# Performance work log

Hardware: AMD Instinct MI355X
Metric: run time of the kernel (lower is better)

## Reference

```python
import jax, jax.numpy as jnp
import numpy as np

D = 2048      # attn_dim
H = 16        # num_heads
HD = D // H   # head_dim = 128
FF = 8192     # ffn_dim
BASE = 10000.0
EPS = 1e-6


def setup_inputs() -> dict:
    key = jax.random.key(0)
    ks = jax.random.split(key, 10)
    b, t = 2, 2048
    s = 1.0 / np.sqrt(D)
    x = jax.random.normal(ks[0], (b, t, D), dtype=jnp.float32)
    position_ids = jnp.arange(b * t, dtype=jnp.int64).reshape(b, t)  # values < maxlen=4096
    return {
        "x": x,
        "position_ids": position_ids,
        "Wq": jax.random.normal(ks[1], (D, D), jnp.float32) * s,
        "Wk": jax.random.normal(ks[2], (D, D), jnp.float32) * s,
        "Wv": jax.random.normal(ks[3], (D, D), jnp.float32) * s,
        "Wo": jax.random.normal(ks[4], (D, D), jnp.float32) * s,
        "Wg": jax.random.normal(ks[5], (D, FF), jnp.float32) * s,
        "Wu": jax.random.normal(ks[6], (D, FF), jnp.float32) * s,
        "Wd": jax.random.normal(ks[7], (FF, D), jnp.float32) * (1.0 / np.sqrt(FF)),
        "g1": jnp.ones((D,), jnp.float32),
        "g2": jnp.ones((D,), jnp.float32),
    }


def _rmsnorm(x, g):
    return x * jax.lax.rsqrt(jnp.mean(x * x, axis=-1, keepdims=True) + EPS) * g


def _rope_cos_sin(position_ids):
    # get_cos_sin: theta over even dims, then repeat(1, 2) -> (b, t, HD)
    inv_freq = 1.0 / (BASE ** (jnp.arange(0, HD, 2, dtype=jnp.float32) / HD))
    ang = position_ids[..., None].astype(jnp.float32) * inv_freq  # (b, t, HD/2)
    cos = jnp.concatenate([jnp.cos(ang), jnp.cos(ang)], axis=-1)  # (b, t, HD)
    sin = jnp.concatenate([jnp.sin(ang), jnp.sin(ang)], axis=-1)
    return cos, sin


def _rotate_half(x):
    x1, x2 = x[..., : HD // 2], x[..., HD // 2:]
    return jnp.concatenate([-x2, x1], axis=-1)


def _attention(xn, position_ids, Wq, Wk, Wv, Wo):
    b, t, _ = xn.shape
    q = (xn @ Wq).reshape(b, t, H, HD).transpose(0, 2, 1, 3)  # b h t d
    k = (xn @ Wk).reshape(b, t, H, HD).transpose(0, 2, 1, 3)
    v = (xn @ Wv).reshape(b, t, H, HD).transpose(0, 2, 1, 3)
    cos, sin = _rope_cos_sin(position_ids)
    cos = cos[:, None]  # b 1 t d
    sin = sin[:, None]
    q = q * cos + _rotate_half(q) * sin
    k = k * cos + _rotate_half(k) * sin
    scores = jnp.einsum("bhqd,bhkd->bhqk", q, k) / np.sqrt(HD).astype(np.float32)
    causal = jnp.triu(jnp.ones((t, t), dtype=bool), k=1)  # True above diagonal
    scores = jnp.where(causal, jnp.float32(-10000.0), scores)
    attn = jax.nn.softmax(scores, axis=-1)
    o = jnp.einsum("bhqk,bhkd->bhqd", attn, v)
    o = o.transpose(0, 2, 1, 3).reshape(b, t, D)
    return o @ Wo


def reference(x, position_ids, Wq, Wk, Wv, Wo, Wg, Wu, Wd, g1, g2):
    x = x + _attention(_rmsnorm(x, g1), position_ids, Wq, Wk, Wv, Wo)
    h = _rmsnorm(x, g2)
    x = x + (jax.nn.silu(h @ Wg) * (h @ Wu)) @ Wd
    return x
```

## Files before the change

kernel.cpp:

```cpp
#include <hip/hip_runtime.h>
#include <cstdint>

#define D_  2048
#define H_  16
#define HD_ 128
#define FF_ 8192
#define T_  2048
#define B_  2
#define BT_ (B_*T_)
#define NP_ (B_*H_)
#define QKVLD_ (3*D_)

typedef __attribute__((ext_vector_type(8))) _Float16 half8;
typedef __attribute__((ext_vector_type(4))) float   floatx4;

__device__ __forceinline__ void gl_lds16(const void* g, void* l) {
  __builtin_amdgcn_global_load_lds(
      (const __attribute__((address_space(1))) void*)(uintptr_t)g,
      (__attribute__((address_space(3))) void*)(uintptr_t)l,
      16, 0, 0);
}

__global__ void wconv_kernel(const float* __restrict__ W, _Float16* __restrict__ Wt,
                             int K, int N) {
  __shared__ float tile[64][33];
  int n0 = blockIdx.x * 32, k0 = blockIdx.y * 64;
  int tx = threadIdx.x, ty = threadIdx.y;
#pragma unroll
  for (int r = 0; r < 64; r += 8)
    tile[ty + r][tx] = W[(size_t)(k0 + ty + r) * N + n0 + tx];
  __syncthreads();
#pragma unroll
  for (int r = 0; r < 32; r += 8) {
    float a = tile[tx * 2][ty + r], b = tile[tx * 2 + 1][ty + r];
    union { _Float16 h[2]; unsigned u; } cv;
    cv.h[0] = (_Float16)a; cv.h[1] = (_Float16)b;
    ((unsigned*)(Wt + (size_t)(n0 + ty + r) * K + k0))[tx] = cv.u;
  }
}

__global__ void rmsnorm_kernel(const float* __restrict__ x, const float* __restrict__ g,
                               _Float16* __restrict__ out) {
  int row = blockIdx.x, tid = threadIdx.x;
  const float4* xr = (const float4*)(x + (size_t)row * D_);
  float4 v1 = xr[tid], v2 = xr[tid + 256];
  float ss = v1.x*v1.x + v1.y*v1.y + v1.z*v1.z + v1.w*v1.w
           + v2.x*v2.x + v2.y*v2.y + v2.z*v2.z + v2.w*v2.w;
  __shared__ float red[256];
  red[tid] = ss; __syncthreads();
  for (int s = 128; s > 0; s >>= 1) { if (tid < s) red[tid] += red[tid + s]; __syncthreads(); }
  float rs = rsqrtf(red[0] * (1.0f / D_) + 1e-6f);
  float4 ga = ((const float4*)g)[tid], gb = ((const float4*)g)[tid + 256];
  _Float16* orow = out + (size_t)row * D_;
  _Float16 t[4] __attribute__((aligned(8)));
  t[0] = (_Float16)(v1.x * rs * ga.x);
  t[1] = (_Float16)(v1.y * rs * ga.y);
  t[2] = (_Float16)(v1.z * rs * ga.z);
  t[3] = (_Float16)(v1.w * rs * ga.w);
  *(uint2*)(orow + tid * 4) = *(const uint2*)t;
  t[0] = (_Float16)(v2.x * rs * gb.x);
  t[1] = (_Float16)(v2.y * rs * gb.y);
  t[2] = (_Float16)(v2.z * rs * gb.z);
  t[3] = (_Float16)(v2.w * rs * gb.w);
  *(uint2*)(orow + (tid + 256) * 4) = *(const uint2*)t;
}

template<int OUTMODE>
__global__ __launch_bounds__(512, 2) void gemm256(
    const _Float16* __restrict__ A, const _Float16* __restrict__ Bt,
    void* __restrict__ Cv, const float* __restrict__ Res,
    int M, int N, int K, int lda, int ldb, int ldc)
{
  extern __shared__ _Float16 smem[];

  const int gx = gridDim.x, gy = gridDim.y, gz = gridDim.z;
  int pid = (blockIdx.z * gy + blockIdx.y) * gx + blockIdx.x;
  const int qch = (gx * gy * gz) >> 3;
  int lid = (pid & 7) * qch + (pid >> 3);
  const int bx = lid % gx; lid /= gx;
  const int by = lid % gy; const int bz = lid / gy;

  const int tid  = threadIdx.x;
  const int lane = tid & 63;
  const int w    = tid >> 6;
  const int wm   = w >> 2;
  const int wn   = w & 3;
  const int l15  = lane & 15, q4 = lane >> 4;
  const int m0   = by * 256;
  const int n0   = bx * 256;
  const int KP   = K / gz;
  const int koff = bz * KP;
  const int NT   = KP >> 6;

  const int srow8  = lane >> 3;
  const int schunk = (((lane & 7) ^ (srow8 & 7)) << 3);
  const _Float16* AgP = A  + (size_t)(m0 + w * 8 + srow8) * lda + schunk + koff;
  const _Float16* BgP = Bt + (size_t)(n0 + w * 8 + srow8) * ldb + schunk + koff;
  const int ldsW = w * 512;

  const int c0 = ((q4 ^ (l15 & 7)) << 3);
  const int c1 = c0 ^ 32;
  const int arow_e = (wm * 128 + l15) * 64;
  const int brow_e = (wn * 64 + l15) * 64;
  const _Float16* aB[2][2];
  const _Float16* bB[2][2];
  aB[0][0] = smem + arow_e + c0;          aB[0][1] = smem + arow_e + c1;
  aB[1][0] = aB[0][0] + 32768;            aB[1][1] = aB[0][1] + 32768;
  bB[0][0] = smem + 16384 + brow_e + c0;  bB[0][1] = smem + 16384 + brow_e + c1;
  bB[1][0] = bB[0][0] + 32768;            bB[1][1] = bB[0][1] + 32768;

  floatx4 acc[8][4];
#pragma unroll
  for (int i = 0; i < 8; ++i)
#pragma unroll
    for (int j = 0; j < 4; ++j)
#pragma unroll
      for (int r = 0; r < 4; ++r) acc[i][j][r] = 0.0f;

  half8 bf[2][4];
  half8 af0[4], af1[4];

#define STA(S, h, s, KO)                                                     \
  gl_lds16(AgP + (size_t)((h) * 128 + (s) * 64) * lda + (KO),                \
           smem + (S) * 32768 + (h) * 8192 + (s) * 4096 + ldsW)
#define STB(S, h, s, KO)                                                     \
  gl_lds16(BgP + (size_t)((h) * 128 + (s) * 64) * ldb + (KO),                \
           smem + (S) * 32768 + 16384 + (h) * 8192 + (s) * 4096 + ldsW)

#define SB0   __builtin_amdgcn_sched_barrier(0)
#define BARR  __builtin_amdgcn_s_barrier()
#define LGKM0 asm volatile("s_waitcnt lgkmcnt(0)" ::: "memory")

#define RD_B8(S)                                                             \
  { _Pragma("unroll")                                                        \
    for (int j = 0; j < 4; ++j) {                                            \
      bf[0][j] = *(const half8*)(bB[S][0] + j * 1024);                       \
      bf[1][j] = *(const half8*)(bB[S][1] + j * 1024);                       \
    } }
#define RD_A4(S, q, af)                                                      \
  { _Pragma("unroll")                                                        \
    for (int i2 = 0; i2 < 2; ++i2) {                                         \
      af[i2*2+0] = *(const half8*)(aB[S][0] + ((q)*2+i2) * 1024);            \
      af[i2*2+1] = *(const half8*)(aB[S][1] + ((q)*2+i2) * 1024);            \
    } }
#define MFMA_Q(q, af)                                                        \
  { _Pragma("unroll")                                                        \
    for (int kk = 0; kk < 2; ++kk)                                           \
      _Pragma("unroll")                                                      \
      for (int i2 = 0; i2 < 2; ++i2)                                         \
        _Pragma("unroll")                                                    \
        for (int j = 0; j < 4; ++j)                                          \
          acc[(q)*2+i2][j] = __builtin_amdgcn_mfma_f32_16x16x32_f16(         \
              af[i2*2+kk], bf[kk][j], acc[(q)*2+i2][j], 0, 0, 0);            \
  }

#define TILE(S, t, KOA, KOB)                                                 \
  {                                                                          \
    const bool s1 = (t) + 1 < NT, s2 = (t) + 2 < NT;                         \
                                                   \
    RD_B8(S); RD_A4(S, 0, af0);                                              \
    if (s1) { STA((S) ^ 1, 0, 0, KOA); STA((S) ^ 1, 0, 1, KOA); }            \
    asm volatile("s_waitcnt lgkmcnt(8)" ::: "memory");                       \
    SB0; BARR; LGKM0; SB0;                                                   \
    __builtin_amdgcn_s_setprio(1); MFMA_Q(0, af0); __builtin_amdgcn_s_setprio(0); \
    SB0; BARR;                                                               \
                                                           \
    RD_A4(S, 1, af1);                                                        \
    if (s1) { STA((S) ^ 1, 1, 0, KOA); STA((S) ^ 1, 1, 1, KOA); }            \
    SB0; BARR; LGKM0; SB0;                                                   \
    __builtin_amdgcn_s_setprio(1); MFMA_Q(1, af1); __builtin_amdgcn_s_setprio(0); \
    SB0; BARR;                                                               \
                                                           \
    RD_A4(S, 2, af0);                                                        \
    if (s2) { STB(S, 0, 0, KOB); STB(S, 0, 1, KOB); }                        \
    SB0; BARR; LGKM0; SB0;                                                   \
    __builtin_amdgcn_s_setprio(1); MFMA_Q(2, af0); __builtin_amdgcn_s_setprio(0); \
    SB0; BARR;                                                               \
                                                           \
    RD_A4(S, 3, af1);                                                        \
    if (s2) { STB(S, 1, 0, KOB); STB(S, 1, 1, KOB); }                        \
    SB0; BARR; LGKM0; SB0;                                                   \
    __builtin_amdgcn_s_setprio(1); MFMA_Q(3, af1); __builtin_amdgcn_s_setprio(0); \
    SB0;                                                                     \
    if (s2)      asm volatile("s_waitcnt vmcnt(4)" ::: "memory");            \
    else if (s1) asm volatile("s_waitcnt vmcnt(0)" ::: "memory");            \
    BARR;                                                                    \
  }

  STA(0, 0, 0, 0); STA(0, 0, 1, 0); STA(0, 1, 0, 0); STA(0, 1, 1, 0);
  STB(0, 0, 0, 0); STB(0, 0, 1, 0); STB(0, 1, 0, 0); STB(0, 1, 1, 0);
  if (NT > 1) {
    STB(1, 0, 0, 64); STB(1, 0, 1, 64); STB(1, 1, 0, 64); STB(1, 1, 1, 64);
    asm volatile("s_waitcnt vmcnt(4)" ::: "memory");
  } else {
    asm volatile("s_waitcnt vmcnt(0)" ::: "memory");
  }
  BARR;

  for (int t = 0; t < NT; t += 2) {
    TILE(0, t,     64, 128);
    TILE(1, t + 1, 128, 192);
    AgP += 128; BgP += 128;
  }

#undef STA
#undef STB
#undef SB0
#undef BARR
#undef LGKM0
#undef RD_B8
#undef RD_A4
#undef MFMA_Q
#undef TILE

  const int crow0 = m0 + wm * 128 + q4 * 4;
  const int ccol0 = n0 + wn * 64 + l15;
#pragma unroll
  for (int i = 0; i < 8; ++i)
#pragma unroll
    for (int j = 0; j < 4; ++j)
#pragma unroll
      for (int r = 0; r < 4; ++r) {
        size_t o = (size_t)(crow0 + i * 16 + r) * ldc + (ccol0 + j * 16);
        if constexpr (OUTMODE == 0)      ((_Float16*)Cv)[o] = (_Float16)acc[i][j][r];
        else if constexpr (OUTMODE == 1) ((float*)Cv)[o] = acc[i][j][r] + Res[o];
        else ((float*)Cv)[(size_t)bz * M * ldc + o] = acc[i][j][r];
      }
}

__global__ void addred_kernel(const float* __restrict__ parts, const float* __restrict__ res,
                              float* __restrict__ out) {
  size_t i = ((size_t)blockIdx.x * 256 + threadIdx.x) * 4;
  const size_t MN = (size_t)BT_ * D_;
  float4 a = *(const float4*)(parts + i);
  float4 b = *(const float4*)(parts + MN + i);
  float4 r = *(const float4*)(res + i);
  float4 o;
  o.x = a.x + b.x + r.x; o.y = a.y + b.y + r.y;
  o.z = a.z + b.z + r.z; o.w = a.w + b.w + r.w;
  *(float4*)(out + i) = o;
}

__global__ __launch_bounds__(256, 2) void fattn_kernel(
    const _Float16* __restrict__ qkv, const _Float16* __restrict__ vt,
    _Float16* __restrict__ ob)
{
  __shared__ _Float16 Pl[128 * 136];
  const int pr = blockIdx.x;
  const int yq = blockIdx.y;
  const int b = pr >> 4, h = pr & 15;
  const int lane = threadIdx.x & 63, w = threadIdx.x >> 6;
  const int l15 = lane & 15, q4 = lane >> 4;
  const float scale = 0.08838834764831845f;

  const _Float16* qg = qkv + (size_t)b * T_ * QKVLD_ + (size_t)h * HD_;
  const _Float16* kg = qg + D_;
  const _Float16* vg = vt + (size_t)pr * HD_ * T_;
  _Float16* og = ob + (size_t)b * T_ * D_ + (size_t)h * HD_;

  for (int hf = 0; hf < 2; ++hf) {
    const int qb = hf ? (15 - yq) : yq;
    const int qrow0 = qb * 128 + w * 32;

    half8 qf[2][4];
#pragma unroll
    for (int i = 0; i < 2; ++i)
#pragma unroll
      for (int kf = 0; kf < 4; ++kf)
        qf[i][kf] = *(const half8*)(qg + (size_t)(qrow0 + i * 16 + l15) * QKVLD_
                                       + kf * 32 + q4 * 8);

    floatx4 Oa[2][8];
    float m[8], l[8];
#pragma unroll
    for (int i = 0; i < 2; ++i)
#pragma unroll
      for (int j = 0; j < 8; ++j)
#pragma unroll
        for (int r = 0; r < 4; ++r) Oa[i][j][r] = 0.f;
#pragma unroll
    for (int z = 0; z < 8; ++z) { m[z] = -1e30f; l[z] = 0.f; }

    for (int kt = 0; kt <= qb; ++kt) {
      floatx4 s[2][8];
#pragma unroll
      for (int i = 0; i < 2; ++i)
#pragma unroll
        for (int j = 0; j < 8; ++j)
#pragma unroll
          for (int r = 0; r < 4; ++r) s[i][j][r] = 0.f;
#pragma unroll
      for (int kf = 0; kf < 4; ++kf) {
#pragma unroll
        for (int j = 0; j < 8; ++j) {
          half8 kf8 = *(const half8*)(kg + (size_t)(kt * 128 + j * 16 + l15) * QKVLD_
                                         + kf * 32 + q4 * 8);
          s[0][j] = __builtin_amdgcn_mfma_f32_16x16x32_f16(qf[0][kf], kf8, s[0][j], 0, 0, 0);
          s[1][j] = __builtin_amdgcn_mfma_f32_16x16x32_f16(qf[1][kf], kf8, s[1][j], 0, 0, 0);
        }
      }
#pragma unroll
      for (int i = 0; i < 2; ++i)
#pragma unroll
        for (int j = 0; j < 8; ++j)
#pragma unroll
          for (int r = 0; r < 4; ++r) s[i][j][r] *= scale;
      if (kt == qb) {
#pragma unroll
        for (int i = 0; i < 2; ++i)
#pragma unroll
          for (int j = 0; j < 8; ++j)
#pragma unroll
            for (int r = 0; r < 4; ++r)
              if (j * 16 + l15 > w * 32 + i * 16 + q4 * 4 + r) s[i][j][r] = -1e30f;
      }
#pragma unroll
      for (int i = 0; i < 2; ++i)
#pragma unroll
        for (int r = 0; r < 4; ++r) {
          const int z = i * 4 + r;
          float pm = s[i][0][r];
#pragma unroll
          for (int j = 1; j < 8; ++j) pm = fmaxf(pm, s[i][j][r]);
          pm = fmaxf(pm, __shfl_xor(pm, 1));
          pm = fmaxf(pm, __shfl_xor(pm, 2));
          pm = fmaxf(pm, __shfl_xor(pm, 4));
          pm = fmaxf(pm, __shfl_xor(pm, 8));
          float mn = fmaxf(m[z], pm);
          float sc = __expf(m[z] - mn);
          m[z] = mn;
          float ls = 0.f;
#pragma unroll
          for (int j = 0; j < 8; ++j) {
            float e = __expf(s[i][j][r] - mn);
            s[i][j][r] = e;
            ls += e;
          }
          ls += __shfl_xor(ls, 1);
          ls += __shfl_xor(ls, 2);
          ls += __shfl_xor(ls, 4);
          ls += __shfl_xor(ls, 8);
          l[z] = l[z] * sc + ls;
#pragma unroll
          for (int jd = 0; jd < 8; ++jd) Oa[i][jd][r] *= sc;
        }
#pragma unroll
      for (int i = 0; i < 2; ++i)
#pragma unroll
        for (int r = 0; r < 4; ++r) {
          _Float16* prow = &Pl[(size_t)(w * 32 + i * 16 + q4 * 4 + r) * 136 + l15];
#pragma unroll
          for (int j = 0; j < 8; ++j) prow[j * 16] = (_Float16)s[i][j][r];
        }
#pragma unroll
      for (int ks = 0; ks < 4; ++ks) {
        half8 pf0 = *(const half8*)&Pl[(size_t)(w * 32 + l15) * 136 + ks * 32 + q4 * 8];
        half8 pf1 = *(const half8*)&Pl[(size_t)(w * 32 + 16 + l15) * 136 + ks * 32 + q4 * 8];
#pragma unroll
        for (int jd = 0; jd < 8; ++jd) {
          half8 vf = *(const half8*)(vg + (size_t)(jd * 16 + l15) * T_
                                        + kt * 128 + ks * 32 + q4 * 8);
          Oa[0][jd] = __builtin_amdgcn_mfma_f32_16x16x32_f16(pf0, vf, Oa[0][jd], 0, 0, 0);
          Oa[1][jd] = __builtin_amdgcn_mfma_f32_16x16x32_f16(pf1, vf, Oa[1][jd], 0, 0, 0);
        }
      }
    }
#pragma unroll
    for (int i = 0; i < 2; ++i)
#pragma unroll
      for (int r = 0; r < 4; ++r) {
        float inv = 1.0f / l[i * 4 + r];
        _Float16* orow = og + (size_t)(qrow0 + i * 16 + q4 * 4 + r) * D_;
#pragma unroll
        for (int jd = 0; jd < 8; ++jd)
          orow[jd * 16 + l15] = (_Float16)(Oa[i][jd][r] * inv);
      }
  }
}

__global__ void rope_kernel(_Float16* __restrict__ qkv, const void* __restrict__ pos) {
  int gid = blockIdx.x * 256 + threadIdx.x;
  int d = gid & 63;
  int h = (gid >> 6) & 15;
  int bt = gid >> 10;
  const int* pi = (const int*)pos;
  long long pv = (pi[1] == 0 && pi[2] == 1) ? ((const long long*)pos)[bt]
                                            : (long long)pi[bt];
  float inv = exp2f((float)d * -0.2076205059304601f);
  float ang = (float)pv * inv;
  float s, c;
  sincosf(ang, &s, &c);
  size_t base = (size_t)bt * QKVLD_ + (size_t)h * HD_ + d;
  _Float16* q = qkv;
  _Float16* k = qkv + D_;
  float x1v = (float)q[base], x2v = (float)q[base + 64];
  q[base]      = (_Float16)(x1v * c - x2v * s);
  q[base + 64] = (_Float16)(x2v * c + x1v * s);
  x1v = (float)k[base]; x2v = (float)k[base + 64];
  k[base]      = (_Float16)(x1v * c - x2v * s);
  k[base + 64] = (_Float16)(x2v * c + x1v * s);
}

__global__ void vtrans_kernel(const _Float16* __restrict__ v, _Float16* __restrict__ vt,
                              int ld) {
  __shared__ _Float16 tile[32][33];
  int t0 = blockIdx.x * 32, d0 = blockIdx.y * 32, bh = blockIdx.z;
  int b = bh >> 4, h = bh & 15;
  int tx = threadIdx.x, ty = threadIdx.y;
  const _Float16* vb = v + (size_t)b * T_ * ld + (size_t)h * HD_;
#pragma unroll
  for (int r = 0; r < 32; r += 8)
    tile[ty + r][tx] = vb[(size_t)(t0 + ty + r) * ld + d0 + tx];
  __syncthreads();
  _Float16* vo = vt + ((size_t)bh * HD_ + d0) * T_ + t0;
#pragma unroll
  for (int r = 0; r < 32; r += 8)
    vo[(size_t)(ty + r) * T_ + tx] = tile[tx][ty + r];
}

__global__ void silumul_kernel(_Float16* __restrict__ gate, const _Float16* __restrict__ up) {
  size_t idx = ((size_t)blockIdx.x * 256 + threadIdx.x) * 8;
  uint4 gr = *(const uint4*)(gate + idx);
  uint4 ur = *(const uint4*)(up + idx);
  const _Float16* gh = (const _Float16*)&gr;
  const _Float16* uh = (const _Float16*)&ur;
  _Float16 t[8] __attribute__((aligned(16)));
#pragma unroll
  for (int l = 0; l < 8; l++) {
    float x = (float)gh[l];
    float s = x / (1.0f + __expf(-x));
    t[l] = (_Float16)(s * (float)uh[l]);
  }
  *(uint4*)(gate + idx) = *(const uint4*)t;
}

extern "C" void kernel_launch(void* const* d_in, const int* in_sizes, int n_in,
                              void* d_out, int out_size, void* d_ws, size_t ws_size,
                              hipStream_t stream) {
  (void)in_sizes; (void)n_in; (void)out_size;
  const float* x   = (const float*)d_in[0];
  const void*  pos = d_in[1];
  const float* W[7] = { (const float*)d_in[2], (const float*)d_in[3],
                        (const float*)d_in[4], (const float*)d_in[5],
                        (const float*)d_in[6], (const float*)d_in[7],
                        (const float*)d_in[8] };
  const float* g1  = (const float*)d_in[9];
  const float* g2  = (const float*)d_in[10];
  float* out = (float*)d_out;

  const int wk[7] = { D_, D_, D_, D_, D_, D_, FF_ };
  const int wn[7] = { D_, D_, D_, D_, FF_, FF_, D_ };

  char* p = (char*)d_ws;
  auto carve = [&](size_t bytes) { char* r = p; p += (bytes + 255) & ~(size_t)255; return r; };

  _Float16* scratch = (_Float16*)carve((size_t)64 * 1024 * 1024);
  const size_t FLAT_NEED = (size_t)336 * 1024 * 1024;
  bool flat = ws_size >= FLAT_NEED;
  _Float16* w16[7];
  if (flat) {
    for (int i = 0; i < 7; i++) w16[i] = (_Float16*)carve((size_t)wk[i] * wn[i] * 2);
  } else {
    _Float16* wslot = (_Float16*)carve((size_t)D_ * FF_ * 2);
    w16[0] = wslot;
    w16[1] = wslot + (size_t)D_ * D_;
    w16[2] = wslot + (size_t)2 * D_ * D_;
    w16[3] = w16[4] = w16[5] = w16[6] = wslot;
  }
  _Float16* qkv = (_Float16*)carve((size_t)BT_ * QKVLD_ * 2);
  _Float16* ob  = (_Float16*)carve((size_t)BT_ * D_ * 2);
  _Float16* xn  = (_Float16*)carve((size_t)BT_ * D_ * 2);
  _Float16* vt  = (_Float16*)carve((size_t)BT_ * D_ * 2);
  float*    x1  = (float*)   carve((size_t)BT_ * D_ * 4);
  _Float16* gate = scratch;
  _Float16* up   = qkv;
  _Float16* hb   = xn;
  float* oparts = (float*)scratch;
  float* dparts = (float*)qkv;

  dim3 b328(32, 8);
  auto conv = [&](int i) {
    wconv_kernel<<<dim3(wn[i] / 32, wk[i] / 64), b328, 0, stream>>>(W[i], w16[i], wk[i], wn[i]);
  };
  if (flat) for (int i = 0; i < 7; i++) conv(i);

  rmsnorm_kernel<<<BT_, 256, 0, stream>>>(x, g1, xn);

  if (!flat) { conv(0); conv(1); conv(2); }
  gemm256<0><<<dim3(QKVLD_ / 256, BT_ / 256, 1), 512, 131072, stream>>>(
      xn, w16[0], qkv, nullptr, BT_, QKVLD_, D_, D_, D_, QKVLD_);

  rope_kernel<<<(BT_ * H_ * 64) / 256, 256, 0, stream>>>(qkv, pos);

  vtrans_kernel<<<dim3(T_ / 32, HD_ / 32, NP_), b328, 0, stream>>>(qkv + 2 * D_, vt, QKVLD_);

  fattn_kernel<<<dim3(NP_, 8), 256, 0, stream>>>(qkv, vt, ob);

  if (!flat) conv(3);
  gemm256<2><<<dim3(D_ / 256, BT_ / 256, 2), 512, 131072, stream>>>(
      ob, w16[3], oparts, nullptr, BT_, D_, D_, D_, D_, D_);
  addred_kernel<<<(BT_ * D_ / 4) / 256, 256, 0, stream>>>(oparts, x, x1);

  rmsnorm_kernel<<<BT_, 256, 0, stream>>>(x1, g2, hb);

  if (!flat) conv(4);
  gemm256<0><<<dim3(FF_ / 256, BT_ / 256, 1), 512, 131072, stream>>>(
      hb, w16[4], gate, nullptr, BT_, FF_, D_, D_, D_, FF_);
  if (!flat) conv(5);
  gemm256<0><<<dim3(FF_ / 256, BT_ / 256, 1), 512, 131072, stream>>>(
      hb, w16[5], up, nullptr, BT_, FF_, D_, D_, D_, FF_);

  silumul_kernel<<<(BT_ * FF_ / 8) / 256, 256, 0, stream>>>(gate, up);

  if (!flat) conv(6);
  gemm256<2><<<dim3(D_ / 256, BT_ / 256, 2), 512, 131072, stream>>>(
      gate, w16[6], dparts, nullptr, BT_, D_, FF_, FF_, FF_, D_);
  addred_kernel<<<(BT_ * D_ / 4) / 256, 256, 0, stream>>>(dparts, x1, out);
}
```

Baseline: 1.179 ms.

## Split attention q-blocks across blocks and double-buffer K/V register loads

Each attention workgroup now handles a single 128-row query block instead of a causal-balanced pair. This doubles the grid to 16 blocks in y (512 workgroups) for more parallelism on the GPU. The K and V fragment loads are software-pipelined into two register buffers, so the next k-slice is fetched while the current MFMAs run, hiding global-load latency. The cost is higher register pressure from the extra half8 buffers, which may reduce occupancy, and uneven per-block work under the causal mask.

```diff
diff --git a/kernel.cpp b/kernel.cpp
--- a/kernel.cpp
+++ b/kernel.cpp
@@ -248,6 +248,7 @@
   __shared__ _Float16 Pl[128 * 136];
   const int pr = blockIdx.x;
   const int yq = blockIdx.y;
+  const int qb = (yq < 8) ? yq : 23 - yq;
   const int b = pr >> 4, h = pr & 15;
   const int lane = threadIdx.x & 63, w = threadIdx.x >> 6;
   const int l15 = lane & 15, q4 = lane >> 4;
@@ -258,124 +259,143 @@
   const _Float16* vg = vt + (size_t)pr * HD_ * T_;
   _Float16* og = ob + (size_t)b * T_ * D_ + (size_t)h * HD_;
 
-  for (int hf = 0; hf < 2; ++hf) {
-    const int qb = hf ? (15 - yq) : yq;
-    const int qrow0 = qb * 128 + w * 32;
-
-    half8 qf[2][4];
+  const int qrow0 = qb * 128 + w * 32;
+
+  half8 qf[2][4];
+#pragma unroll
+  for (int i = 0; i < 2; ++i)
+#pragma unroll
+    for (int kf = 0; kf < 4; ++kf)
+      qf[i][kf] = *(const half8*)(qg + (size_t)(qrow0 + i * 16 + l15) * QKVLD_
+                                     + kf * 32 + q4 * 8);
+
+  floatx4 Oa[2][8];
+  float m[8], l[8];
+#pragma unroll
+  for (int i = 0; i < 2; ++i)
+#pragma unroll
+    for (int j = 0; j < 8; ++j)
+#pragma unroll
+      for (int r = 0; r < 4; ++r) Oa[i][j][r] = 0.f;
+#pragma unroll
+  for (int z = 0; z < 8; ++z) { m[z] = -1e30f; l[z] = 0.f; }
+
+  for (int kt = 0; kt <= qb; ++kt) {
+    const _Float16* kb_ = kg + (size_t)(kt * 128 + l15) * QKVLD_ + q4 * 8;
+    half8 k0[8], k1[8];
+#pragma unroll
+    for (int j = 0; j < 8; ++j)
+      k0[j] = *(const half8*)(kb_ + (size_t)(j * 16) * QKVLD_);
+    floatx4 s[2][8];
 #pragma unroll
     for (int i = 0; i < 2; ++i)
 #pragma unroll
-      for (int kf = 0; kf < 4; ++kf)
-        qf[i][kf] = *(const half8*)(qg + (size_t)(qrow0 + i * 16 + l15) * QKVLD_
-                                       + kf * 32 + q4 * 8);
-
-    floatx4 Oa[2][8];
-    float m[8], l[8];
+      for (int j = 0; j < 8; ++j)
+#pragma unroll
+        for (int r = 0; r < 4; ++r) s[i][j][r] = 0.f;
+#pragma unroll
+    for (int kf = 0; kf < 4; ++kf) {
+      if (kf < 3) {
+#pragma unroll
+        for (int j = 0; j < 8; ++j) {
+          half8 nx = *(const half8*)(kb_ + (size_t)(j * 16) * QKVLD_ + (kf + 1) * 32);
+          if (kf & 1) k0[j] = nx; else k1[j] = nx;
+        }
+      }
+#pragma unroll
+      for (int j = 0; j < 8; ++j) {
+        half8 cur = (kf & 1) ? k1[j] : k0[j];
+        s[0][j] = __builtin_amdgcn_mfma_f32_16x16x32_f16(qf[0][kf], cur, s[0][j], 0, 0, 0);
+        s[1][j] = __builtin_amdgcn_mfma_f32_16x16x32_f16(qf[1][kf], cur, s[1][j], 0, 0, 0);
+      }
+    }
 #pragma unroll
     for (int i = 0; i < 2; ++i)
 #pragma unroll
       for (int j = 0; j < 8; ++j)
 #pragma unroll
-        for (int r = 0; r < 4; ++r) Oa[i][j][r] = 0.f;
-#pragma unroll
-    for (int z = 0; z < 8; ++z) { m[z] = -1e30f; l[z] = 0.f; }
-
-    for (int kt = 0; kt <= qb; ++kt) {
-      floatx4 s[2][8];
+        for (int r = 0; r < 4; ++r) s[i][j][r] *= scale;
+    if (kt == qb) {
 #pragma unroll
       for (int i = 0; i < 2; ++i)
 #pragma unroll
         for (int j = 0; j < 8; ++j)
 #pragma unroll
-          for (int r = 0; r < 4; ++r) s[i][j][r] = 0.f;
-#pragma unroll
-      for (int kf = 0; kf < 4; ++kf) {
+          for (int r = 0; r < 4; ++r)
+            if (j * 16 + l15 > w * 32 + i * 16 + q4 * 4 + r) s[i][j][r] = -1e30f;
+    }
+    const _Float16* vb_ = vg + (size_t)(l15) * T_ + kt * 128 + q4 * 8;
+    half8 v0[8], v1[8];
+#pragma unroll
+    for (int jd = 0; jd < 8; ++jd)
+      v0[jd] = *(const half8*)(vb_ + (size_t)(jd * 16) * T_);
+#pragma unroll
+    for (int i = 0; i < 2; ++i)
+#pragma unroll
+      for (int r = 0; r < 4; ++r) {
+        const int z = i * 4 + r;
+        float pm = s[i][0][r];
+#pragma unroll
+        for (int j = 1; j < 8; ++j) pm = fmaxf(pm, s[i][j][r]);
+        pm = fmaxf(pm, __shfl_xor(pm, 1));
+        pm = fmaxf(pm, __shfl_xor(pm, 2));
+        pm = fmaxf(pm, __shfl_xor(pm, 4));
+        pm = fmaxf(pm, __shfl_xor(pm, 8));
+        float mn = fmaxf(m[z], pm);
+        float sc = __expf(m[z] - mn);
+        m[z] = mn;
+        float ls = 0.f;
 #pragma unroll
         for (int j = 0; j < 8; ++j) {
-          half8 kf8 = *(const half8*)(kg + (size_t)(kt * 128 + j * 16 + l15) * QKVLD_
-                                         + kf * 32 + q4 * 8);
-          s[0][j] = __builtin_amdgcn_mfma_f32_16x16x32_f16(qf[0][kf], kf8, s[0][j], 0, 0, 0);
-          s[1][j] = __builtin_amdgcn_mfma_f32_16x16x32_f16(qf[1][kf], kf8, s[1][j], 0, 0, 0);
+          float e = __expf(s[i][j][r] - mn);
+          s[i][j][r] = e;
+          ls += e;
         }
-      }
-#pragma unroll
-      for (int i = 0; i < 2; ++i)
-#pragma unroll
-        for (int j = 0; j < 8; ++j)
-#pragma unroll
-          for (int r = 0; r < 4; ++r) s[i][j][r] *= scale;
-      if (kt == qb) {
-#pragma unroll
-        for (int i = 0; i < 2; ++i)
-#pragma unroll
-          for (int j = 0; j < 8; ++j)
-#pragma unroll
-            for (int r = 0; r < 4; ++r)
-              if (j * 16 + l15 > w * 32 + i * 16 + q4 * 4 + r) s[i][j][r] = -1e30f;
-      }
-#pragma unroll
-      for (int i = 0; i < 2; ++i)
-#pragma unroll
-        for (int r = 0; r < 4; ++r) {
-          const int z = i * 4 + r;
-          float pm = s[i][0][r];
-#pragma unroll
-          for (int j = 1; j < 8; ++j) pm = fmaxf(pm, s[i][j][r]);
-          pm = fmaxf(pm, __shfl_xor(pm, 1));
-          pm = fmaxf(pm, __shfl_xor(pm, 2));
-          pm = fmaxf(pm, __shfl_xor(pm, 4));
-          pm = fmaxf(pm, __shfl_xor(pm, 8));
-          float mn = fmaxf(m[z], pm);
-          float sc = __expf(m[z] - mn);
-          m[z] = mn;
-          float ls = 0.f;
-#pragma unroll
-          for (int j = 0; j < 8; ++j) {
-            float e = __expf(s[i][j][r] - mn);
-            s[i][j][r] = e;
-            ls += e;
-          }
-          ls += __shfl_xor(ls, 1);
-          ls += __shfl_xor(ls, 2);
-          ls += __shfl_xor(ls, 4);
-          ls += __shfl_xor(ls, 8);
-          l[z] = l[z] * sc + ls;
-#pragma unroll
-          for (int jd = 0; jd < 8; ++jd) Oa[i][jd][r] *= sc;
+        ls += __shfl_xor(ls, 1);
+        ls += __shfl_xor(ls, 2);
+        ls += __shfl_xor(ls, 4);
+        ls += __shfl_xor(ls, 8);
+        l[z] = l[z] * sc + ls;
+#pragma unroll
+        for (int jd = 0; jd < 8; ++jd) Oa[i][jd][r] *= sc;
+      }
+#pragma unroll
+    for (int i = 0; i < 2; ++i)
+#pragma unroll
+      for (int r = 0; r < 4; ++r) {
+        _Float16* prow = &Pl[(size_t)(w * 32 + i * 16 + q4 * 4 + r) * 136 + l15];
+#pragma unroll
+        for (int j = 0; j < 8; ++j) prow[j * 16] = (_Float16)s[i][j][r];
+      }
+#pragma unroll
+    for (int ks = 0; ks < 4; ++ks) {
+      if (ks < 3) {
+#pragma unroll
+        for (int jd = 0; jd < 8; ++jd) {
+          half8 nx = *(const half8*)(vb_ + (size_t)(jd * 16) * T_ + (ks + 1) * 32);
+          if (ks & 1) v0[jd] = nx; else v1[jd] = nx;
         }
-#pragma unroll
-      for (int i = 0; i < 2; ++i)
-#pragma unroll
-        for (int r = 0; r < 4; ++r) {
-          _Float16* prow = &Pl[(size_t)(w * 32 + i * 16 + q4 * 4 + r) * 136 + l15];
-#pragma unroll
-          for (int j = 0; j < 8; ++j) prow[j * 16] = (_Float16)s[i][j][r];
-        }
-#pragma unroll
-      for (int ks = 0; ks < 4; ++ks) {
-        half8 pf0 = *(const half8*)&Pl[(size_t)(w * 32 + l15) * 136 + ks * 32 + q4 * 8];
-        half8 pf1 = *(const half8*)&Pl[(size_t)(w * 32 + 16 + l15) * 136 + ks * 32 + q4 * 8];
-#pragma unroll
-        for (int jd = 0; jd < 8; ++jd) {
-          half8 vf = *(const half8*)(vg + (size_t)(jd * 16 + l15) * T_
-                                        + kt * 128 + ks * 32 + q4 * 8);
-          Oa[0][jd] = __builtin_amdgcn_mfma_f32_16x16x32_f16(pf0, vf, Oa[0][jd], 0, 0, 0);
-          Oa[1][jd] = __builtin_amdgcn_mfma_f32_16x16x32_f16(pf1, vf, Oa[1][jd], 0, 0, 0);
-        }
+      }
+      half8 pf0 = *(const half8*)&Pl[(size_t)(w * 32 + l15) * 136 + ks * 32 + q4 * 8];
+      half8 pf1 = *(const half8*)&Pl[(size_t)(w * 32 + 16 + l15) * 136 + ks * 32 + q4 * 8];
+#pragma unroll
+      for (int jd = 0; jd < 8; ++jd) {
+        half8 vf = (ks & 1) ? v1[jd] : v0[jd];
+        Oa[0][jd] = __builtin_amdgcn_mfma_f32_16x16x32_f16(pf0, vf, Oa[0][jd], 0, 0, 0);
+        Oa[1][jd] = __builtin_amdgcn_mfma_f32_16x16x32_f16(pf1, vf, Oa[1][jd], 0, 0, 0);
       }
     }
-#pragma unroll
-    for (int i = 0; i < 2; ++i)
-#pragma unroll
-      for (int r = 0; r < 4; ++r) {
-        float inv = 1.0f / l[i * 4 + r];
-        _Float16* orow = og + (size_t)(qrow0 + i * 16 + q4 * 4 + r) * D_;
-#pragma unroll
-        for (int jd = 0; jd < 8; ++jd)
-          orow[jd * 16 + l15] = (_Float16)(Oa[i][jd][r] * inv);
-      }
-  }
+  }
+#pragma unroll
+  for (int i = 0; i < 2; ++i)
+#pragma unroll
+    for (int r = 0; r < 4; ++r) {
+      float inv = 1.0f / l[i * 4 + r];
+      _Float16* orow = og + (size_t)(qrow0 + i * 16 + q4 * 4 + r) * D_;
+#pragma unroll
+      for (int jd = 0; jd < 8; ++jd)
+        orow[jd * 16 + l15] = (_Float16)(Oa[i][jd][r] * inv);
+    }
 }
 
 __global__ void rope_kernel(_Float16* __restrict__ qkv, const void* __restrict__ pos) {
@@ -494,7 +514,7 @@
 
   vtrans_kernel<<<dim3(T_ / 32, HD_ / 32, NP_), b328, 0, stream>>>(qkv + 2 * D_, vt, QKVLD_);
 
-  fattn_kernel<<<dim3(NP_, 8), 256, 0, stream>>>(qkv, vt, ob);
+  fattn_kernel<<<dim3(NP_, 16), 256, 0, stream>>>(qkv, vt, ob);
 
   if (!flat) conv(3);
   gemm256<2><<<dim3(D_ / 256, BT_ / 256, 2), 512, 131072, stream>>>(
```

Result: faster. 1.134 ms (-3.8%).

## Restructure flash attention into 64-row query blocks with software-prefetched K/V fragments

Applied to the files above, without the earlier changes.

The attention kernel now gives each block 64 query rows (16 per wave) instead of pairing two 128-row blocks, and launches 32 query blocks per head-batch pair, heaviest first. Per-thread register state is halved so launch bounds can allow 4 blocks per CU. K and V fragments are prefetched in two halves so global loads overlap with the MFMAs. K/V tiles are still re-read from global memory per block, so total K/V traffic doubles in exchange for more parallelism and occupancy.

```diff
diff --git a/kernel.cpp b/kernel.cpp
--- a/kernel.cpp
+++ b/kernel.cpp
@@ -241,13 +241,14 @@
   *(float4*)(out + i) = o;
 }
 
-__global__ __launch_bounds__(256, 2) void fattn_kernel(
+__global__ __launch_bounds__(256, 4) void fattn_kernel(
     const _Float16* __restrict__ qkv, const _Float16* __restrict__ vt,
     _Float16* __restrict__ ob)
 {
-  __shared__ _Float16 Pl[128 * 136];
+  __shared__ _Float16 Pl[64 * 136];
   const int pr = blockIdx.x;
-  const int yq = blockIdx.y;
+  const int qb = 31 - (int)blockIdx.y;
+  const int nt = (qb + 2) >> 1;
   const int b = pr >> 4, h = pr & 15;
   const int lane = threadIdx.x & 63, w = threadIdx.x >> 6;
   const int l15 = lane & 15, q4 = lane >> 4;
@@ -258,123 +259,125 @@
   const _Float16* vg = vt + (size_t)pr * HD_ * T_;
   _Float16* og = ob + (size_t)b * T_ * D_ + (size_t)h * HD_;
 
-  for (int hf = 0; hf < 2; ++hf) {
-    const int qb = hf ? (15 - yq) : yq;
-    const int qrow0 = qb * 128 + w * 32;
-
-    half8 qf[2][4];
-#pragma unroll
-    for (int i = 0; i < 2; ++i)
-#pragma unroll
-      for (int kf = 0; kf < 4; ++kf)
-        qf[i][kf] = *(const half8*)(qg + (size_t)(qrow0 + i * 16 + l15) * QKVLD_
-                                       + kf * 32 + q4 * 8);
-
-    floatx4 Oa[2][8];
-    float m[8], l[8];
-#pragma unroll
-    for (int i = 0; i < 2; ++i)
+  const int qrow0 = qb * 64 + w * 16;
+
+  half8 qf[4];
+#pragma unroll
+  for (int kf = 0; kf < 4; ++kf)
+    qf[kf] = *(const half8*)(qg + (size_t)(qrow0 + l15) * QKVLD_ + kf * 32 + q4 * 8);
+
+  floatx4 Oa[8];
+  float m[4], l[4];
+#pragma unroll
+  for (int j = 0; j < 8; ++j)
+#pragma unroll
+    for (int r = 0; r < 4; ++r) Oa[j][r] = 0.f;
+#pragma unroll
+  for (int z = 0; z < 4; ++z) { m[z] = -1e30f; l[z] = 0.f; }
+
+  for (int kt = 0; kt < nt; ++kt) {
+    const _Float16* kb_ = kg + (size_t)(kt * 128 + l15) * QKVLD_ + q4 * 8;
+    half8 ka[4], kc[4];
+#pragma unroll
+    for (int j = 0; j < 4; ++j)
+      ka[j] = *(const half8*)(kb_ + (size_t)(j * 16) * QKVLD_);
+    floatx4 s[8];
+#pragma unroll
+    for (int j = 0; j < 8; ++j)
+#pragma unroll
+      for (int r = 0; r < 4; ++r) s[j][r] = 0.f;
+#pragma unroll
+    for (int kf = 0; kf < 4; ++kf) {
+#pragma unroll
+      for (int j = 0; j < 4; ++j)
+        kc[j] = *(const half8*)(kb_ + (size_t)((j + 4) * 16) * QKVLD_ + kf * 32);
+#pragma unroll
+      for (int j = 0; j < 4; ++j)
+        s[j] = __builtin_amdgcn_mfma_f32_16x16x32_f16(qf[kf], ka[j], s[j], 0, 0, 0);
+      if (kf < 3) {
+#pragma unroll
+        for (int j = 0; j < 4; ++j)
+          ka[j] = *(const half8*)(kb_ + (size_t)(j * 16) * QKVLD_ + (kf + 1) * 32);
+      }
+#pragma unroll
+      for (int j = 0; j < 4; ++j)
+        s[4 + j] = __builtin_amdgcn_mfma_f32_16x16x32_f16(qf[kf], kc[j], s[4 + j], 0, 0, 0);
+    }
+#pragma unroll
+    for (int j = 0; j < 8; ++j)
+#pragma unroll
+      for (int r = 0; r < 4; ++r) s[j][r] *= scale;
+    if (kt == nt - 1) {
 #pragma unroll
       for (int j = 0; j < 8; ++j)
 #pragma unroll
-        for (int r = 0; r < 4; ++r) Oa[i][j][r] = 0.f;
-#pragma unroll
-    for (int z = 0; z < 8; ++z) { m[z] = -1e30f; l[z] = 0.f; }
-
-    for (int kt = 0; kt <= qb; ++kt) {
-      floatx4 s[2][8];
-#pragma unroll
-      for (int i = 0; i < 2; ++i)
-#pragma unroll
-        for (int j = 0; j < 8; ++j)
-#pragma unroll
-          for (int r = 0; r < 4; ++r) s[i][j][r] = 0.f;
-#pragma unroll
-      for (int kf = 0; kf < 4; ++kf) {
-#pragma unroll
-        for (int j = 0; j < 8; ++j) {
-          half8 kf8 = *(const half8*)(kg + (size_t)(kt * 128 + j * 16 + l15) * QKVLD_
-                                         + kf * 32 + q4 * 8);
-          s[0][j] = __builtin_amdgcn_mfma_f32_16x16x32_f16(qf[0][kf], kf8, s[0][j], 0, 0, 0);
-          s[1][j] = __builtin_amdgcn_mfma_f32_16x16x32_f16(qf[1][kf], kf8, s[1][j], 0, 0, 0);
-        }
+        for (int r = 0; r < 4; ++r)
+          if (kt * 128 + j * 16 + l15 > qrow0 + q4 * 4 + r) s[j][r] = -1e30f;
+    }
+    const _Float16* vb_ = vg + (size_t)l15 * T_ + kt * 128 + q4 * 8;
+    half8 va[4], vc[4];
+#pragma unroll
+    for (int jd = 0; jd < 4; ++jd)
+      va[jd] = *(const half8*)(vb_ + (size_t)(jd * 16) * T_);
+#pragma unroll
+    for (int r = 0; r < 4; ++r) {
+      float pm = s[0][r];
+#pragma unroll
+      for (int j = 1; j < 8; ++j) pm = fmaxf(pm, s[j][r]);
+      pm = fmaxf(pm, __shfl_xor(pm, 1));
+      pm = fmaxf(pm, __shfl_xor(pm, 2));
+      pm = fmaxf(pm, __shfl_xor(pm, 4));
+      pm = fmaxf(pm, __shfl_xor(pm, 8));
+      float mn = fmaxf(m[r], pm);
+      float sc = __expf(m[r] - mn);
+      m[r] = mn;
+      float ls = 0.f;
+#pragma unroll
+      for (int j = 0; j < 8; ++j) {
+        float e = __expf(s[j][r] - mn);
+        s[j][r] = e;
+        ls += e;
       }
-#pragma unroll
-      for (int i = 0; i < 2; ++i)
-#pragma unroll
-        for (int j = 0; j < 8; ++j)
-#pragma unroll
-          for (int r = 0; r < 4; ++r) s[i][j][r] *= scale;
-      if (kt == qb) {
-#pragma unroll
-        for (int i = 0; i < 2; ++i)
-#pragma unroll
-          for (int j = 0; j < 8; ++j)
-#pragma unroll
-            for (int r = 0; r < 4; ++r)
-              if (j * 16 + l15 > w * 32 + i * 16 + q4 * 4 + r) s[i][j][r] = -1e30f;
+      ls += __shfl_xor(ls, 1);
+      ls += __shfl_xor(ls, 2);
+      ls += __shfl_xor(ls, 4);
+      ls += __shfl_xor(ls, 8);
+      l[r] = l[r] * sc + ls;
+#pragma unroll
+      for (int jd = 0; jd < 8; ++jd) Oa[jd][r] *= sc;
+    }
+#pragma unroll
+    for (int r = 0; r < 4; ++r) {
+      _Float16* prow = &Pl[(size_t)(w * 16 + q4 * 4 + r) * 136 + l15];
+#pragma unroll
+      for (int j = 0; j < 8; ++j) prow[j * 16] = (_Float16)s[j][r];
+    }
+#pragma unroll
+    for (int ks = 0; ks < 4; ++ks) {
+#pragma unroll
+      for (int jd = 0; jd < 4; ++jd)
+        vc[jd] = *(const half8*)(vb_ + (size_t)((jd + 4) * 16) * T_ + ks * 32);
+      half8 pf = *(const half8*)&Pl[(size_t)(w * 16 + l15) * 136 + ks * 32 + q4 * 8];
+#pragma unroll
+      for (int jd = 0; jd < 4; ++jd)
+        Oa[jd] = __builtin_amdgcn_mfma_f32_16x16x32_f16(pf, va[jd], Oa[jd], 0, 0, 0);
+      if (ks < 3) {
+#pragma unroll
+        for (int jd = 0; jd < 4; ++jd)
+          va[jd] = *(const half8*)(vb_ + (size_t)(jd * 16) * T_ + (ks + 1) * 32);
       }
 #pragma unroll
-      for (int i = 0; i < 2; ++i)
-#pragma unroll
-        for (int r = 0; r < 4; ++r) {
-          const int z = i * 4 + r;
-          float pm = s[i][0][r];
-#pragma unroll
-          for (int j = 1; j < 8; ++j) pm = fmaxf(pm, s[i][j][r]);
-          pm = fmaxf(pm, __shfl_xor(pm, 1));
-          pm = fmaxf(pm, __shfl_xor(pm, 2));
-          pm = fmaxf(pm, __shfl_xor(pm, 4));
-          pm = fmaxf(pm, __shfl_xor(pm, 8));
-          float mn = fmaxf(m[z], pm);
-          float sc = __expf(m[z] - mn);
-          m[z] = mn;
-          float ls = 0.f;
-#pragma unroll
-          for (int j = 0; j < 8; ++j) {
-            float e = __expf(s[i][j][r] - mn);
-            s[i][j][r] = e;
-            ls += e;
-          }
-          ls += __shfl_xor(ls, 1);
-          ls += __shfl_xor(ls, 2);
-          ls += __shfl_xor(ls, 4);
-          ls += __shfl_xor(ls, 8);
-          l[z] = l[z] * sc + ls;
-#pragma unroll
-          for (int jd = 0; jd < 8; ++jd) Oa[i][jd][r] *= sc;
-        }
-#pragma unroll
-      for (int i = 0; i < 2; ++i)
-#pragma unroll
-        for (int r = 0; r < 4; ++r) {
-          _Float16* prow = &Pl[(size_t)(w * 32 + i * 16 + q4 * 4 + r) * 136 + l15];
-#pragma unroll
-          for (int j = 0; j < 8; ++j) prow[j * 16] = (_Float16)s[i][j][r];
-        }
-#pragma unroll
-      for (int ks = 0; ks < 4; ++ks) {
-        half8 pf0 = *(const half8*)&Pl[(size_t)(w * 32 + l15) * 136 + ks * 32 + q4 * 8];
-        half8 pf1 = *(const half8*)&Pl[(size_t)(w * 32 + 16 + l15) * 136 + ks * 32 + q4 * 8];
-#pragma unroll
-        for (int jd = 0; jd < 8; ++jd) {
-          half8 vf = *(const half8*)(vg + (size_t)(jd * 16 + l15) * T_
-                                        + kt * 128 + ks * 32 + q4 * 8);
-          Oa[0][jd] = __builtin_amdgcn_mfma_f32_16x16x32_f16(pf0, vf, Oa[0][jd], 0, 0, 0);
-          Oa[1][jd] = __builtin_amdgcn_mfma_f32_16x16x32_f16(pf1, vf, Oa[1][jd], 0, 0, 0);
-        }
-      }
+      for (int jd = 0; jd < 4; ++jd)
+        Oa[4 + jd] = __builtin_amdgcn_mfma_f32_16x16x32_f16(pf, vc[jd], Oa[4 + jd], 0, 0, 0);
     }
-#pragma unroll
-    for (int i = 0; i < 2; ++i)
-#pragma unroll
-      for (int r = 0; r < 4; ++r) {
-        float inv = 1.0f / l[i * 4 + r];
-        _Float16* orow = og + (size_t)(qrow0 + i * 16 + q4 * 4 + r) * D_;
-#pragma unroll
-        for (int jd = 0; jd < 8; ++jd)
-          orow[jd * 16 + l15] = (_Float16)(Oa[i][jd][r] * inv);
-      }
+  }
+#pragma unroll
+  for (int r = 0; r < 4; ++r) {
+    float inv = 1.0f / l[r];
+    _Float16* orow = og + (size_t)(qrow0 + q4 * 4 + r) * D_;
+#pragma unroll
+    for (int jd = 0; jd < 8; ++jd)
+      orow[jd * 16 + l15] = (_Float16)(Oa[jd][r] * inv);
   }
 }
 
@@ -494,7 +497,7 @@
 
   vtrans_kernel<<<dim3(T_ / 32, HD_ / 32, NP_), b328, 0, stream>>>(qkv + 2 * D_, vt, QKVLD_);
 
-  fattn_kernel<<<dim3(NP_, 8), 256, 0, stream>>>(qkv, vt, ob);
+  fattn_kernel<<<dim3(NP_, 32), 256, 0, stream>>>(qkv, vt, ob);
 
   if (!flat) conv(3);
   gemm256<2><<<dim3(D_ / 256, BT_ / 256, 2), 512, 131072, stream>>>(
```

Result: slower. 1.242 ms (+5.4%).
